# Optimization experiments

Measured on AMD Instinct MI355X. Metric: run time of the kernel, lower is better.

## Reference

```python
import jax, jax.numpy as jnp
import numpy as np

EPS = 1e-8
NUM_ITERATIONS = 3


def layer_norm(x, g, b, eps=EPS):
    m = jnp.mean(x, axis=-1, keepdims=True)
    v = jnp.mean((x - m) ** 2, axis=-1, keepdims=True)
    return (x - m) * jax.lax.rsqrt(v + eps) * g + b


def gru_cell(x, h, w_ih, w_hh, b_ih, b_hh):
    # PyTorch GRUCell: gates ordered (r, z, n)
    gi = x @ w_ih.T + b_ih  # [B*S, 3D]
    gh = h @ w_hh.T + b_hh
    i_r, i_z, i_n = jnp.split(gi, 3, axis=-1)
    h_r, h_z, h_n = jnp.split(gh, 3, axis=-1)
    r = jax.nn.sigmoid(i_r + h_r)
    z = jax.nn.sigmoid(i_z + h_z)
    n = jnp.tanh(i_n + r * h_n)
    return (1.0 - z) * n + z * h


def setup_inputs() -> dict:
    key = jax.random.key(0)
    ks = jax.random.split(key, 12)
    B, N, D, S = 64, 1024, 512, 16
    s = 1.0 / np.sqrt(D)
    return {
        "inputs": jax.random.normal(ks[0], (B, N, D), jnp.float32),
        "noise": jax.random.normal(ks[1], (B, S, D), jnp.float32),
        "slot_mu": jax.random.normal(ks[2], (1, 1, D), jnp.float32),
        "slot_log_sigma": jnp.zeros((1, 1, D), jnp.float32),
        "ln_in_g": jnp.ones((D,), jnp.float32),
        "ln_in_b": jnp.zeros((D,), jnp.float32),
        "ln_slots_g": jnp.ones((D,), jnp.float32),
        "ln_slots_b": jnp.zeros((D,), jnp.float32),
        "ln_mlp_g": jnp.ones((D,), jnp.float32),
        "ln_mlp_b": jnp.zeros((D,), jnp.float32),
        "Wq": jax.random.normal(ks[3], (D, D), jnp.float32) * s,
        "Wk": jax.random.normal(ks[4], (D, D), jnp.float32) * s,
        "Wv": jax.random.normal(ks[5], (D, D), jnp.float32) * s,
        "gru_w_ih": jax.random.normal(ks[6], (3 * D, D), jnp.float32) * s,
        "gru_w_hh": jax.random.normal(ks[7], (3 * D, D), jnp.float32) * s,
        "gru_b_ih": jnp.zeros((3 * D,), jnp.float32),
        "gru_b_hh": jnp.zeros((3 * D,), jnp.float32),
        "mlp_w1": jax.random.normal(ks[8], (D, D), jnp.float32) * s,
        "mlp_b1": jnp.zeros((D,), jnp.float32),
        "mlp_w2": jax.random.normal(ks[9], (D, D), jnp.float32) * s,
        "mlp_b2": jnp.zeros((D,), jnp.float32),
    }


def reference(inputs, noise, slot_mu, slot_log_sigma,
              ln_in_g, ln_in_b, ln_slots_g, ln_slots_b, ln_mlp_g, ln_mlp_b,
              Wq, Wk, Wv, gru_w_ih, gru_w_hh, gru_b_ih, gru_b_hh,
              mlp_w1, mlp_b1, mlp_w2, mlp_b2):
    B, N, D = inputs.shape
    S = noise.shape[1]
    scale = D ** (-0.5)

    # slot init: mu + sigma * eps
    slots = slot_mu + jnp.exp(slot_log_sigma) * noise  # [B,S,D]

    x = layer_norm(inputs, ln_in_g, ln_in_b)
    k = x @ Wk.T  # [B,N,D]
    v = x @ Wv.T

    for _ in range(NUM_ITERATIONS):
        slots_prev = slots
        sn = layer_norm(slots, ln_slots_g, ln_slots_b)
        q = sn @ Wq.T  # [B,S,D]
        attn_logits = jnp.einsum("bnd,bmd->bnm", q, k) * scale  # [B,S,N]
        attn = jax.nn.softmax(attn_logits, axis=-1)
        attn = attn / (jnp.sum(attn, axis=1, keepdims=True) + EPS)  # column-normalize over slots
        updates = jnp.einsum("bnm,bmd->bnd", attn, v)  # [B,S,D]
        slots = gru_cell(updates.reshape(-1, D), slots_prev.reshape(-1, D),
                         gru_w_ih, gru_w_hh, gru_b_ih, gru_b_hh).reshape(B, S, D)
        h = jax.nn.relu(layer_norm(slots, ln_mlp_g, ln_mlp_b) @ mlp_w1.T + mlp_b1)
        slots = slots + h @ mlp_w2.T + mlp_b2

    # proj_to_hidden is Identity (slot_dim == hidden_size); forward_dtype=float32
    return slots
```

## Files before the change

kernel.cpp:

```cpp
#include <hip/hip_runtime.h>
#include <hip/hip_bf16.h>
#include <cstdint>
#include <cstddef>


typedef __bf16 bf16x8 __attribute__((ext_vector_type(8)));
typedef float f32x4 __attribute__((ext_vector_type(4)));

__device__ __forceinline__ float bf2f(unsigned int u) {
  union { unsigned int i; float f; } v; v.i = u << 16; return v.f;
}
__device__ __forceinline__ unsigned short f2bf(float x) {
  __hip_bfloat16 h = __float2bfloat16(x);
  unsigned short u;
  __builtin_memcpy(&u, &h, 2);
  return u;
}

#define GLD16(gp, lp)                                                       \
  __builtin_amdgcn_global_load_lds(                                         \
      (const __attribute__((address_space(1))) void*)(gp),                  \
      (__attribute__((address_space(3))) void*)(lp), 16, 0, 0)


__global__ void wprep_k(const float* __restrict__ w1, const float* __restrict__ w2,
                        const float* __restrict__ wih, const float* __restrict__ bih,
                        const float* __restrict__ bhh, const float* __restrict__ mu,
                        const float* __restrict__ ls, const float* __restrict__ noise,
                        unsigned short* __restrict__ w1_bf, unsigned short* __restrict__ w2_bf,
                        unsigned short* __restrict__ wih_bf, float* __restrict__ bcat,
                        float* __restrict__ slots) {
  int blk = blockIdx.x, t = threadIdx.x;
  if (blk < 1024) {
    int i = blk * 256 + t; w1_bf[i] = f2bf(w1[i]);
  } else if (blk < 2048) {
    int i = (blk - 1024) * 256 + t; w2_bf[i] = f2bf(w2[i]);
  } else if (blk < 5120) {
    int i = (blk - 2048) * 256 + t; wih_bf[i] = f2bf(wih[i]);
  } else if (blk < 5128) {
    int j = (blk - 5120) * 256 + t;
    float v;
    if (j < 1024)      v = bih[j] + bhh[j];
    else if (j < 1536) v = bih[j];
    else               v = bhh[j - 512];
    bcat[j] = v;
  } else {
    int i = (blk - 5128) * 256 + t;
    int d = i & 511;
    slots[i] = mu[d] + expf(ls[d]) * noise[i];
  }
}

__global__ void wcat_k(const float* __restrict__ wihp, const float* __restrict__ whh,
                       unsigned short* __restrict__ out) {
  int i = blockIdx.x * 256 + threadIdx.x;
  int j = i >> 10, k = i & 1023;
  float v;
  if (j < 1024)      v = (k < 512) ? wihp[j * 512 + k] : whh[j * 512 + (k - 512)];
  else if (j < 1536) v = (k < 512) ? wihp[j * 512 + k] : 0.0f;
  else               v = (k < 512) ? 0.0f : whh[(j - 512) * 512 + (k - 512)];
  out[i] = f2bf(v);
}

__global__ __launch_bounds__(256) void tcast3_k(const float* __restrict__ Wq,
                                                const float* __restrict__ Wk,
                                                const float* __restrict__ Wv,
                                                unsigned short* __restrict__ wqT,
                                                unsigned short* __restrict__ wkT,
                                                unsigned short* __restrict__ wvT) {
  __shared__ float tt[32][33];
  const float* in = blockIdx.z == 0 ? Wq : (blockIdx.z == 1 ? Wk : Wv);
  unsigned short* out = blockIdx.z == 0 ? wqT : (blockIdx.z == 1 ? wkT : wvT);
  int c0 = blockIdx.x << 5, r0 = blockIdx.y << 5;
  int tx = threadIdx.x & 31, ty = threadIdx.x >> 5;
  #pragma unroll
  for (int i = 0; i < 4; ++i)
    tt[ty + 8 * i][tx] = in[(size_t)(r0 + ty + 8 * i) * 512 + c0 + tx];
  __syncthreads();
  #pragma unroll
  for (int i = 0; i < 4; ++i)
    out[(size_t)(c0 + ty + 8 * i) * 512 + r0 + tx] = f2bf(tt[tx][ty + 8 * i]);
}


__global__ __launch_bounds__(256) void ln_rows_k(
    const float* __restrict__ in, const float* __restrict__ g, const float* __restrict__ b,
    unsigned short* __restrict__ out, int rows) {
  int w = threadIdx.x >> 6, lane = threadIdx.x & 63;
  int row = (blockIdx.x << 2) + w;
  if (row >= rows) return;
  const float4* rp = reinterpret_cast<const float4*>(in + (size_t)row * 512);
  float4 v0 = rp[lane], v1 = rp[lane + 64];
  float s = v0.x + v0.y + v0.z + v0.w + v1.x + v1.y + v1.z + v1.w;
  float q = v0.x*v0.x + v0.y*v0.y + v0.z*v0.z + v0.w*v0.w
          + v1.x*v1.x + v1.y*v1.y + v1.z*v1.z + v1.w*v1.w;
  #pragma unroll
  for (int o = 32; o > 0; o >>= 1) { s += __shfl_xor(s, o); q += __shfl_xor(q, o); }
  float m = s * (1.0f / 512.0f);
  float rstd = rsqrtf(q * (1.0f / 512.0f) - m * m + 1e-8f);
  const float4* gp = reinterpret_cast<const float4*>(g);
  const float4* bp = reinterpret_cast<const float4*>(b);
  float4 g0 = gp[lane], g1 = gp[lane + 64];
  float4 b0 = bp[lane], b1 = bp[lane + 64];
  ushort4 o0, o1;
  o0.x = f2bf((v0.x - m) * rstd * g0.x + b0.x);
  o0.y = f2bf((v0.y - m) * rstd * g0.y + b0.y);
  o0.z = f2bf((v0.z - m) * rstd * g0.z + b0.z);
  o0.w = f2bf((v0.w - m) * rstd * g0.w + b0.w);
  o1.x = f2bf((v1.x - m) * rstd * g1.x + b1.x);
  o1.y = f2bf((v1.y - m) * rstd * g1.y + b1.y);
  o1.z = f2bf((v1.z - m) * rstd * g1.z + b1.z);
  o1.w = f2bf((v1.w - m) * rstd * g1.w + b1.w);
  ushort4* op = reinterpret_cast<ushort4*>(out + (size_t)row * 512);
  op[lane] = o0; op[lane + 64] = o1;
}


__global__ __launch_bounds__(256) void xt_k(const unsigned short* __restrict__ x,
                                            unsigned short* __restrict__ xT) {
  __shared__ unsigned short t[64][68];
  int nt = blockIdx.x, et = blockIdx.y, b = blockIdx.z;
  int r = threadIdx.x >> 3, c8 = (threadIdx.x & 7) << 3;
  #pragma unroll
  for (int p = 0; p < 2; ++p) {
    int row = r + (p << 5);
    *reinterpret_cast<uint4*>(&t[row][c8]) = *reinterpret_cast<const uint4*>(
        x + ((size_t)(b << 10) + (nt << 6) + row) * 512 + (et << 6) + c8);
  }
  __syncthreads();
  #pragma unroll
  for (int p = 0; p < 2; ++p) {
    int erow = r + (p << 5);
    ushort4 a, bb;
    #pragma unroll
    for (int j = 0; j < 4; ++j) ((unsigned short*)&a)[j] = t[c8 + j][erow];
    #pragma unroll
    for (int j = 0; j < 4; ++j) ((unsigned short*)&bb)[j] = t[c8 + 4 + j][erow];
    unsigned short* o = xT + ((size_t)(b << 9) + (et << 6) + erow) * 1024 + (nt << 6) + c8;
    *reinterpret_cast<ushort4*>(o) = a;
    *reinterpret_cast<ushort4*>(o + 4) = bb;
  }
}

__global__ __launch_bounds__(256) void gru_ln_k(
    const float* __restrict__ gates, const float* __restrict__ hp,
    const float* __restrict__ g, const float* __restrict__ b,
    float* __restrict__ sgru, unsigned short* __restrict__ lnm) {
  int w = threadIdx.x >> 6, lane = threadIdx.x & 63;
  int row = (blockIdx.x << 2) + w;
  size_t gb = (size_t)row * 2048 + (lane << 3);
  size_t hb = (size_t)row * 512 + (lane << 3);
  float rs[8], zs[8], in_[8], hn[8], hv[8], y[8];
  #pragma unroll
  for (int c = 0; c < 2; ++c) {
    *reinterpret_cast<float4*>(rs + 4*c)  = *reinterpret_cast<const float4*>(gates + gb + 4*c);
    *reinterpret_cast<float4*>(zs + 4*c)  = *reinterpret_cast<const float4*>(gates + gb + 512 + 4*c);
    *reinterpret_cast<float4*>(in_ + 4*c) = *reinterpret_cast<const float4*>(gates + gb + 1024 + 4*c);
    *reinterpret_cast<float4*>(hn + 4*c)  = *reinterpret_cast<const float4*>(gates + gb + 1536 + 4*c);
    *reinterpret_cast<float4*>(hv + 4*c)  = *reinterpret_cast<const float4*>(hp + hb + 4*c);
  }
  float s = 0.f, q = 0.f;
  #pragma unroll
  for (int j = 0; j < 8; ++j) {
    float r = 1.0f / (1.0f + expf(-rs[j]));
    float z = 1.0f / (1.0f + expf(-zs[j]));
    float n = tanhf(in_[j] + r * hn[j]);
    float h = (1.0f - z) * n + z * hv[j];
    y[j] = h; s += h; q += h * h;
  }
  #pragma unroll
  for (int o = 32; o > 0; o >>= 1) { s += __shfl_xor(s, o); q += __shfl_xor(q, o); }
  float m = s * (1.0f / 512.0f);
  float rstd = rsqrtf(q * (1.0f / 512.0f) - m * m + 1e-8f);
  const float* gg = g + (lane << 3);
  const float* bb = b + (lane << 3);
  #pragma unroll
  for (int c = 0; c < 2; ++c)
    *reinterpret_cast<float4*>(sgru + hb + 4*c) = *reinterpret_cast<const float4*>(y + 4*c);
  uint4 o4;
  unsigned int p[8];
  #pragma unroll
  for (int j = 0; j < 8; ++j) p[j] = f2bf((y[j] - m) * rstd * gg[j] + bb[j]);
  o4.x = p[0] | (p[1] << 16); o4.y = p[2] | (p[3] << 16);
  o4.z = p[4] | (p[5] << 16); o4.w = p[6] | (p[7] << 16);
  *reinterpret_cast<uint4*>(lnm + hb) = o4;
}


template<int OUTBF16>
__global__ __launch_bounds__(256) void gemm_bt(
    const unsigned short* __restrict__ A, const unsigned short* __restrict__ W,
    void* __restrict__ Cout, int M, int N, int K) {
  __shared__ unsigned short sA[2][4096];
  __shared__ unsigned short sB[2][4096];
  const int tid = threadIdx.x;
  const int lane = tid & 63, w = tid >> 6;

  int nwg = gridDim.x * gridDim.y;
  int flat = blockIdx.y * gridDim.x + blockIdx.x;
  if ((nwg & 7) == 0) { int c = nwg >> 3; flat = (flat & 7) * c + (flat >> 3); }
  const int row0 = (flat / gridDim.x) << 7;
  const int col0 = (flat % gridDim.x) << 7;

  const int wm = (w >> 1) << 6, wn = (w & 1) << 6;
  const int lrow = lane & 15, kt = (lane >> 4) << 3;
  const int srow = lane >> 2, scol = (lane & 3) << 3;

  f32x4 acc[4][4];
  #pragma unroll
  for (int m = 0; m < 4; ++m)
    #pragma unroll
    for (int n = 0; n < 4; ++n) acc[m][n] = f32x4{0.f, 0.f, 0.f, 0.f};

  auto stage = [&](int buf, int k0) {
    #pragma unroll
    for (int i = 0; i < 2; ++i) {
      int ii = w * 2 + i;
      int r = (ii << 4) + srow;
      GLD16(A + (size_t)(row0 + r) * K + k0 + scol, &sA[buf][ii * 512]);
      GLD16(W + (size_t)(col0 + r) * K + k0 + scol, &sB[buf][ii * 512]);
    }
  };

  stage(0, 0);
  const int nt = K >> 5;
  int cur = 0;
  for (int t = 0; t < nt; ++t) {
    __syncthreads();
    if (t + 1 < nt) stage(cur ^ 1, (t + 1) << 5);
    bf16x8 af[4], bfv[4];
    #pragma unroll
    for (int m = 0; m < 4; ++m)
      af[m] = *reinterpret_cast<const bf16x8*>(&sA[cur][(wm + m * 16 + lrow) * 32 + kt]);
    #pragma unroll
    for (int n = 0; n < 4; ++n)
      bfv[n] = *reinterpret_cast<const bf16x8*>(&sB[cur][(wn + n * 16 + lrow) * 32 + kt]);
    #pragma unroll
    for (int m = 0; m < 4; ++m)
      #pragma unroll
      for (int n = 0; n < 4; ++n)
        acc[m][n] = __builtin_amdgcn_mfma_f32_16x16x32_bf16(af[m], bfv[n], acc[m][n], 0, 0, 0);
    cur ^= 1;
  }

  const int rb = (lane >> 4) << 2;
  #pragma unroll
  for (int m = 0; m < 4; ++m) {
    #pragma unroll
    for (int n = 0; n < 4; ++n) {
      int col = col0 + wn + n * 16 + lrow;
      #pragma unroll
      for (int r = 0; r < 4; ++r) {
        int row = row0 + wm + m * 16 + rb + r;
        float v = acc[m][n][r];
        if (OUTBF16) ((unsigned short*)Cout)[(size_t)row * N + col] = f2bf(v);
        else ((float*)Cout)[(size_t)row * N + col] = v;
      }
    }
  }
}


__global__ __launch_bounds__(256) void q2ln_k(
    const float* __restrict__ slots, const float* __restrict__ g, const float* __restrict__ b,
    const unsigned short* __restrict__ wpt, unsigned short* __restrict__ q2,
    unsigned short* __restrict__ A2) {
  __shared__ unsigned short s_sn[16 * 520];
  __shared__ unsigned short sB[2][4096];
  const int b_ = blockIdx.y, ct = blockIdx.x;
  const int lane = threadIdx.x & 63, w = threadIdx.x >> 6;
  const int lrow = lane & 15, kt = (lane >> 4) << 3;
  const int srow = lane >> 2, scol = (lane & 3) << 3;

  const float4* gp = reinterpret_cast<const float4*>(g);
  const float4* bp = reinterpret_cast<const float4*>(b);
  float4 g0 = gp[lane], g1 = gp[lane + 64];
  float4 b0 = bp[lane], b1 = bp[lane + 64];
  #pragma unroll
  for (int rr = 0; rr < 4; ++rr) {
    int r = w * 4 + rr;
    const float4* rp = reinterpret_cast<const float4*>(slots + (size_t)(b_ * 16 + r) * 512);
    float4 v0 = rp[lane], v1 = rp[lane + 64];
    float s = v0.x + v0.y + v0.z + v0.w + v1.x + v1.y + v1.z + v1.w;
    float q = v0.x*v0.x + v0.y*v0.y + v0.z*v0.z + v0.w*v0.w
            + v1.x*v1.x + v1.y*v1.y + v1.z*v1.z + v1.w*v1.w;
    #pragma unroll
    for (int o = 32; o > 0; o >>= 1) { s += __shfl_xor(s, o); q += __shfl_xor(q, o); }
    float m = s * (1.0f / 512.0f);
    float rstd = rsqrtf(q * (1.0f / 512.0f) - m * m + 1e-8f);
    ushort4 o0, o1;
    o0.x = f2bf((v0.x - m) * rstd * g0.x + b0.x);
    o0.y = f2bf((v0.y - m) * rstd * g0.y + b0.y);
    o0.z = f2bf((v0.z - m) * rstd * g0.z + b0.z);
    o0.w = f2bf((v0.w - m) * rstd * g0.w + b0.w);
    o1.x = f2bf((v1.x - m) * rstd * g1.x + b1.x);
    o1.y = f2bf((v1.y - m) * rstd * g1.y + b1.y);
    o1.z = f2bf((v1.z - m) * rstd * g1.z + b1.z);
    o1.w = f2bf((v1.w - m) * rstd * g1.w + b1.w);
    *reinterpret_cast<ushort4*>(&s_sn[r * 520 + lane * 4]) = o0;
    *reinterpret_cast<ushort4*>(&s_sn[r * 520 + 256 + lane * 4]) = o1;
    if (ct == 0) {
      ushort4 c0, c1;
      c0.x = f2bf(v0.x); c0.y = f2bf(v0.y); c0.z = f2bf(v0.z); c0.w = f2bf(v0.w);
      c1.x = f2bf(v1.x); c1.y = f2bf(v1.y); c1.z = f2bf(v1.z); c1.w = f2bf(v1.w);
      unsigned short* a2r = A2 + (size_t)(b_ * 16 + r) * 1024 + 512;
      *reinterpret_cast<ushort4*>(a2r + lane * 4) = c0;
      *reinterpret_cast<ushort4*>(a2r + 256 + lane * 4) = c1;
    }
  }

  const unsigned short* Bb = wpt + (size_t)(ct << 7) * 512;
  auto stage = [&](int buf, int k0) {
    #pragma unroll
    for (int i = 0; i < 2; ++i) {
      int ii = w * 2 + i;
      GLD16(Bb + (size_t)((ii << 4) + srow) * 512 + k0 + scol, &sB[buf][ii * 512]);
    }
  };

  f32x4 acc[2];
  acc[0] = f32x4{0.f, 0.f, 0.f, 0.f};
  acc[1] = f32x4{0.f, 0.f, 0.f, 0.f};

  stage(0, 0);
  int cur = 0;
  for (int t = 0; t < 16; ++t) {
    __syncthreads();
    if (t + 1 < 16) stage(cur ^ 1, (t + 1) << 5);
    bf16x8 af = *reinterpret_cast<const bf16x8*>(&s_sn[lrow * 520 + (t << 5) + kt]);
    #pragma unroll
    for (int ni = 0; ni < 2; ++ni) {
      bf16x8 bfv = *reinterpret_cast<const bf16x8*>(&sB[cur][((w * 2 + ni) * 16 + lrow) * 32 + kt]);
      acc[ni] = __builtin_amdgcn_mfma_f32_16x16x32_bf16(af, bfv, acc[ni], 0, 0, 0);
    }
    cur ^= 1;
  }

  const int rb = (lane >> 4) << 2;
  #pragma unroll
  for (int ni = 0; ni < 2; ++ni) {
    int col = (ct << 7) + (w * 2 + ni) * 16 + lrow;
    #pragma unroll
    for (int r = 0; r < 4; ++r) {
      int s = rb + r;
      q2[(size_t)((b_ << 4) + s) * 512 + col] = f2bf(acc[ni][r]);
    }
  }
}


__global__ __launch_bounds__(256) void logits_k(
    const unsigned short* __restrict__ q2, const unsigned short* __restrict__ x,
    unsigned short* __restrict__ out) {
  __shared__ unsigned short sA[2][512];
  __shared__ unsigned short sB[2][4096];
  const int b = blockIdx.y, nt = blockIdx.x;
  const int lane = threadIdx.x & 63, w = threadIdx.x >> 6;
  const int lrow = lane & 15, kt = (lane >> 4) << 3;
  const int srow = lane >> 2, scol = (lane & 3) << 3;
  const unsigned short* Ab = q2 + ((size_t)b << 13);
  const unsigned short* Bb = x + (((size_t)(b << 10) + (nt << 7)) << 9);

  f32x4 acc[2];
  acc[0] = f32x4{0.f, 0.f, 0.f, 0.f};
  acc[1] = f32x4{0.f, 0.f, 0.f, 0.f};

  auto stage = [&](int buf, int k0) {
    #pragma unroll
    for (int i = 0; i < 2; ++i) {
      int ii = w * 2 + i;
      GLD16(Bb + (size_t)((ii << 4) + srow) * 512 + k0 + scol, &sB[buf][ii * 512]);
    }
    if (w == 0)
      GLD16(Ab + (size_t)srow * 512 + k0 + scol, &sA[buf][0]);
  };

  stage(0, 0);
  int cur = 0;
  for (int t = 0; t < 16; ++t) {
    __syncthreads();
    if (t + 1 < 16) stage(cur ^ 1, (t + 1) << 5);
    bf16x8 af = *reinterpret_cast<const bf16x8*>(&sA[cur][lrow * 32 + kt]);
    #pragma unroll
    for (int ni = 0; ni < 2; ++ni) {
      bf16x8 bfv = *reinterpret_cast<const bf16x8*>(&sB[cur][((w * 2 + ni) * 16 + lrow) * 32 + kt]);
      acc[ni] = __builtin_amdgcn_mfma_f32_16x16x32_bf16(af, bfv, acc[ni], 0, 0, 0);
    }
    cur ^= 1;
  }

  const int rb = (lane >> 4) << 2;
  #pragma unroll
  for (int ni = 0; ni < 2; ++ni) {
    int n = (nt << 7) + (w * 2 + ni) * 16 + lrow;
    #pragma unroll
    for (int r = 0; r < 4; ++r) {
      int s = rb + r;
      out[(size_t)((b << 4) + s) * 1024 + n] = f2bf(acc[ni][r]);
    }
  }
}


__global__ __launch_bounds__(256) void pv_sm_k(
    const unsigned short* __restrict__ logits, const unsigned short* __restrict__ xT,
    unsigned short* __restrict__ A2) {
  __shared__ float s_mi[16][2];
  __shared__ unsigned short s_at[16 * 1032];
  __shared__ unsigned short sA[2][4096];
  const int b_ = blockIdx.y, et = blockIdx.x;
  const int lane = threadIdx.x & 63, w = threadIdx.x >> 6;
  const int lrow = lane & 15, kt = (lane >> 4) << 3;
  const int srow = lane >> 2, scol = (lane & 3) << 3;
  const unsigned short* lg = logits + ((size_t)b_ << 14);

  #pragma unroll
  for (int rr = 0; rr < 4; ++rr) {
    int r = w * 4 + rr;
    const unsigned short* rp = lg + (size_t)r * 1024;
    float v[16];
    float mx = -3.4e38f;
    #pragma unroll
    for (int i = 0; i < 16; ++i) { v[i] = bf2f(rp[lane + (i << 6)]); mx = fmaxf(mx, v[i]); }
    #pragma unroll
    for (int o = 32; o > 0; o >>= 1) mx = fmaxf(mx, __shfl_xor(mx, o));
    float s = 0.f;
    #pragma unroll
    for (int i = 0; i < 16; ++i) s += __expf(v[i] - mx);
    #pragma unroll
    for (int o = 32; o > 0; o >>= 1) s += __shfl_xor(s, o);
    if (lane == 0) { s_mi[r][0] = mx; s_mi[r][1] = 1.0f / s; }
  }
  __syncthreads();

  #pragma unroll
  for (int j = 0; j < 4; ++j) {
    int c = threadIdx.x + (j << 8);
    float e[16];
    float cs = 0.f;
    #pragma unroll
    for (int s = 0; s < 16; ++s) {
      e[s] = __expf(bf2f(lg[(size_t)s * 1024 + c]) - s_mi[s][0]) * s_mi[s][1];
      cs += e[s];
    }
    float rv = 1.0f / (cs + 1e-8f);
    #pragma unroll
    for (int s = 0; s < 16; ++s) s_at[s * 1032 + c] = f2bf(e[s] * rv);
  }

  const unsigned short* Ab = xT + ((size_t)b_ << 19) + (size_t)(et << 7) * 1024;
  auto stage = [&](int buf, int k0) {
    #pragma unroll
    for (int i = 0; i < 2; ++i) {
      int ii = w * 2 + i;
      GLD16(Ab + (size_t)((ii << 4) + srow) * 1024 + k0 + scol, &sA[buf][ii * 512]);
    }
  };

  f32x4 acc[2];
  acc[0] = f32x4{0.f, 0.f, 0.f, 0.f};
  acc[1] = f32x4{0.f, 0.f, 0.f, 0.f};

  stage(0, 0);
  int cur = 0;
  for (int t = 0; t < 32; ++t) {
    __syncthreads();
    if (t + 1 < 32) stage(cur ^ 1, (t + 1) << 5);
    bf16x8 bfv = *reinterpret_cast<const bf16x8*>(&s_at[lrow * 1032 + (t << 5) + kt]);
    #pragma unroll
    for (int mi = 0; mi < 2; ++mi) {
      bf16x8 af = *reinterpret_cast<const bf16x8*>(&sA[cur][((w * 2 + mi) * 16 + lrow) * 32 + kt]);
      acc[mi] = __builtin_amdgcn_mfma_f32_16x16x32_bf16(af, bfv, acc[mi], 0, 0, 0);
    }
    cur ^= 1;
  }

  const int rb = (lane >> 4) << 2;
  const int s = lrow;
  #pragma unroll
  for (int mi = 0; mi < 2; ++mi) {
    int e0 = (et << 7) + (w * 2 + mi) * 16 + rb;
    ushort4 o;
    o.x = f2bf(acc[mi][0]); o.y = f2bf(acc[mi][1]);
    o.z = f2bf(acc[mi][2]); o.w = f2bf(acc[mi][3]);
    *reinterpret_cast<ushort4*>(&A2[(size_t)((b_ << 4) + s) * 1024 + e0]) = o;
  }
}


template<int BIAS, int RELU, int ADDSRC, int OUTBF16, int SCALE>
__global__ __launch_bounds__(256) void gemm_sm(
    const unsigned short* __restrict__ A, const unsigned short* __restrict__ W,
    const float* __restrict__ bias, const float* __restrict__ addsrc,
    void* __restrict__ Cout, int M, int N, int K, float scalev) {
  __shared__ unsigned short sA[2][2048];
  __shared__ unsigned short sB[2][2048];
  const int tid = threadIdx.x;
  const int lane = tid & 63, w = tid >> 6;

  int nwg = gridDim.x * gridDim.y;
  int flat = blockIdx.y * gridDim.x + blockIdx.x;
  if ((nwg & 7) == 0) { int c = nwg >> 3; flat = (flat & 7) * c + (flat >> 3); }
  const int row0 = (flat / gridDim.x) << 6;
  const int col0 = (flat % gridDim.x) << 6;

  const int lrow = lane & 15, kt = (lane >> 4) << 3;
  const int srow = lane >> 2, scol = (lane & 3) << 3;

  f32x4 acc[4];
  #pragma unroll
  for (int m = 0; m < 4; ++m) acc[m] = f32x4{0.f, 0.f, 0.f, 0.f};

  auto stage = [&](int buf, int k0) {
    int r = (w << 4) + srow;
    GLD16(A + (size_t)(row0 + r) * K + k0 + scol, &sA[buf][w * 512]);
    GLD16(W + (size_t)(col0 + r) * K + k0 + scol, &sB[buf][w * 512]);
  };

  stage(0, 0);
  const int nt = K >> 5;
  int cur = 0;
  for (int t = 0; t < nt; ++t) {
    __syncthreads();
    if (t + 1 < nt) stage(cur ^ 1, (t + 1) << 5);
    bf16x8 af[4], bfv;
    #pragma unroll
    for (int m = 0; m < 4; ++m)
      af[m] = *reinterpret_cast<const bf16x8*>(&sA[cur][(m * 16 + lrow) * 32 + kt]);
    bfv = *reinterpret_cast<const bf16x8*>(&sB[cur][((w << 4) + lrow) * 32 + kt]);
    #pragma unroll
    for (int m = 0; m < 4; ++m)
      acc[m] = __builtin_amdgcn_mfma_f32_16x16x32_bf16(af[m], bfv, acc[m], 0, 0, 0);
    cur ^= 1;
  }

  const int rb = (lane >> 4) << 2;
  const int col = col0 + (w << 4) + lrow;
  float bv = BIAS ? bias[col] : 0.0f;
  #pragma unroll
  for (int m = 0; m < 4; ++m) {
    #pragma unroll
    for (int r = 0; r < 4; ++r) {
      int row = row0 + m * 16 + rb + r;
      float v = acc[m][r];
      if (SCALE) v *= scalev;
      v += bv;
      if (ADDSRC) v += addsrc[(size_t)row * N + col];
      if (RELU) v = fmaxf(v, 0.0f);
      if (OUTBF16) ((unsigned short*)Cout)[(size_t)row * N + col] = f2bf(v);
      else ((float*)Cout)[(size_t)row * N + col] = v;
    }
  }
}


extern "C" void kernel_launch(void* const* d_in, const int* in_sizes, int n_in,
                              void* d_out, int out_size, void* d_ws, size_t ws_size,
                              hipStream_t stream) {
  const float* inputs  = (const float*)d_in[0];
  const float* noise   = (const float*)d_in[1];
  const float* slot_mu = (const float*)d_in[2];
  const float* slot_ls = (const float*)d_in[3];
  const float* ln_in_g = (const float*)d_in[4];
  const float* ln_in_b = (const float*)d_in[5];
  const float* ln_s_g  = (const float*)d_in[6];
  const float* ln_s_b  = (const float*)d_in[7];
  const float* ln_m_g  = (const float*)d_in[8];
  const float* ln_m_b  = (const float*)d_in[9];
  const float* Wq   = (const float*)d_in[10];
  const float* Wk   = (const float*)d_in[11];
  const float* Wv   = (const float*)d_in[12];
  const float* w_ih = (const float*)d_in[13];
  const float* w_hh = (const float*)d_in[14];
  const float* b_ih = (const float*)d_in[15];
  const float* b_hh = (const float*)d_in[16];
  const float* w1   = (const float*)d_in[17];
  const float* b1   = (const float*)d_in[18];
  const float* w2   = (const float*)d_in[19];
  const float* b2   = (const float*)d_in[20];

  const int BN = 65536, BS = 1024;

  uintptr_t base = (uintptr_t)d_ws;
  auto alloc = [&](size_t bytes) {
    void* p = (void*)base;
    base += (bytes + 255) & ~(size_t)255;
    return p;
  };
  unsigned short* x_bf    = (unsigned short*)alloc((size_t)BN * 512 * 2);
  unsigned short* xT      = (unsigned short*)alloc((size_t)64 * 512 * 1024 * 2);
  unsigned short* wqT     = (unsigned short*)alloc(512 * 512 * 2);
  unsigned short* wkT     = (unsigned short*)alloc(512 * 512 * 2);
  unsigned short* wvT     = (unsigned short*)alloc(512 * 512 * 2);
  unsigned short* wpt     = (unsigned short*)alloc(512 * 512 * 2);
  unsigned short* wih_bf  = (unsigned short*)alloc((size_t)1536 * 512 * 2);
  float*          wihp    = (float*)alloc((size_t)1536 * 512 * 4);
  unsigned short* wcat_bf = (unsigned short*)alloc((size_t)2048 * 1024 * 2);
  float*          bcat    = (float*)alloc(2048 * 4);
  unsigned short* w1_bf   = (unsigned short*)alloc(512 * 512 * 2);
  unsigned short* w2_bf   = (unsigned short*)alloc(512 * 512 * 2);
  float*          slots   = (float*)alloc((size_t)BS * 512 * 4);
  unsigned short* A2      = (unsigned short*)alloc((size_t)BS * 1024 * 2);
  unsigned short* q2_bf   = (unsigned short*)alloc((size_t)BS * 512 * 2);
  unsigned short* logits  = (unsigned short*)alloc((size_t)64 * 16 * 1024 * 2);
  float*          gates   = (float*)alloc((size_t)BS * 2048 * 4);
  float*          sgru    = (float*)alloc((size_t)BS * 512 * 4);
  unsigned short* lnm_bf  = (unsigned short*)alloc((size_t)BS * 512 * 2);
  unsigned short* h_bf    = (unsigned short*)alloc((size_t)BS * 512 * 2);
  (void)ws_size; (void)n_in; (void)in_sizes; (void)out_size;

  const float scale = 0.044194173824159216f;

  wprep_k<<<7176, 256, 0, stream>>>(w1, w2, w_ih, b_ih, b_hh, slot_mu, slot_ls, noise,
                                    w1_bf, w2_bf, wih_bf, bcat, slots);
  tcast3_k<<<dim3(16, 16, 3), 256, 0, stream>>>(Wq, Wk, Wv, wqT, wkT, wvT);
  gemm_sm<0,0,0,1,1><<<dim3(8, 8), 256, 0, stream>>>(
      wkT, wqT, nullptr, nullptr, wpt, 512, 512, 512, scale);
  gemm_bt<0><<<dim3(4, 12), 256, 0, stream>>>(
      wih_bf, wvT, wihp, 1536, 512, 512);
  wcat_k<<<8192, 256, 0, stream>>>(wihp, w_hh, wcat_bf);
  ln_rows_k<<<16384, 256, 0, stream>>>(inputs, ln_in_g, ln_in_b, x_bf, BN);
  xt_k<<<dim3(16, 8, 64), 256, 0, stream>>>(x_bf, xT);

  for (int it = 0; it < 3; ++it) {
    q2ln_k<<<dim3(4, 64), 256, 0, stream>>>(slots, ln_s_g, ln_s_b, wpt, q2_bf, A2);
    logits_k<<<dim3(8, 64), 256, 0, stream>>>(q2_bf, x_bf, logits);
    pv_sm_k<<<dim3(4, 64), 256, 0, stream>>>(logits, xT, A2);
    gemm_sm<1,0,0,0,0><<<dim3(32, 16), 256, 0, stream>>>(
        A2, wcat_bf, bcat, nullptr, gates, BS, 2048, 1024, 1.0f);
    gru_ln_k<<<256, 256, 0, stream>>>(gates, slots, ln_m_g, ln_m_b, sgru, lnm_bf);
    gemm_sm<1,1,0,1,0><<<dim3(8, 16), 256, 0, stream>>>(
        lnm_bf, w1_bf, b1, nullptr, h_bf, BS, 512, 512, 1.0f);
    float* slots_out = (it == 2) ? (float*)d_out : slots;
    gemm_sm<1,0,1,0,0><<<dim3(8, 16), 256, 0, stream>>>(
        h_bf, w2_bf, b2, sgru, slots_out, BS, 512, 512, 1.0f);
  }
}
```

Before: 344.0 us.

## Double K-tile depth to 64 in all GEMMs and write Wih·Wv directly into wcat

Every MFMA GEMM kernel now stages 64-wide K tiles instead of 32, which halves the number of barrier/stage iterations and doubles the LDS buffers. The Wih·Wv product now writes bf16 directly into the concatenated GRU weight buffer with a leading dimension. The whh halves and zero blocks of that buffer are filled in the prep kernel, which removes the fp32 intermediate and the separate wcat kernel. Larger LDS use may reduce occupancy, and the 64-wide rows may raise LDS bank conflicts.

```diff
diff --git a/kernel.cpp b/kernel.cpp
--- a/kernel.cpp
+++ b/kernel.cpp
@@ -24,12 +24,13 @@
 
 
 __global__ void wprep_k(const float* __restrict__ w1, const float* __restrict__ w2,
-                        const float* __restrict__ wih, const float* __restrict__ bih,
-                        const float* __restrict__ bhh, const float* __restrict__ mu,
-                        const float* __restrict__ ls, const float* __restrict__ noise,
+                        const float* __restrict__ wih, const float* __restrict__ whh,
+                        const float* __restrict__ bih, const float* __restrict__ bhh,
+                        const float* __restrict__ mu, const float* __restrict__ ls,
+                        const float* __restrict__ noise,
                         unsigned short* __restrict__ w1_bf, unsigned short* __restrict__ w2_bf,
-                        unsigned short* __restrict__ wih_bf, float* __restrict__ bcat,
-                        float* __restrict__ slots) {
+                        unsigned short* __restrict__ wih_bf, unsigned short* __restrict__ wcat,
+                        float* __restrict__ bcat, float* __restrict__ slots) {
   int blk = blockIdx.x, t = threadIdx.x;
   if (blk < 1024) {
     int i = blk * 256 + t; w1_bf[i] = f2bf(w1[i]);
@@ -37,29 +38,36 @@
     int i = (blk - 1024) * 256 + t; w2_bf[i] = f2bf(w2[i]);
   } else if (blk < 5120) {
     int i = (blk - 2048) * 256 + t; wih_bf[i] = f2bf(wih[i]);
-  } else if (blk < 5128) {
-    int j = (blk - 5120) * 256 + t;
+  } else if (blk < 7168) {
+    int i = (blk - 5120) * 256 + t;
+    int j = i >> 9, d = i & 511;
+    wcat[(size_t)j * 1024 + 512 + d] = f2bf(whh[(size_t)j * 512 + d]);
+  } else if (blk < 8192) {
+    int i = (blk - 7168) * 256 + t;
+    int j = i >> 9, d = i & 511;
+    wcat[(size_t)(1536 + j) * 1024 + 512 + d] = f2bf(whh[(size_t)(1024 + j) * 512 + d]);
+  } else if (blk < 10240) {
+    int i = (blk - 8192) * 256 + t;
+    if (i < 262144) {
+      int j = i >> 9, d = i & 511;
+      wcat[(size_t)(1536 + j) * 1024 + d] = 0;
+    } else {
+      int k = i - 262144;
+      int j = k >> 9, d = k & 511;
+      wcat[(size_t)(1024 + j) * 1024 + 512 + d] = 0;
+    }
+  } else if (blk < 10248) {
+    int j = (blk - 10240) * 256 + t;
     float v;
     if (j < 1024)      v = bih[j] + bhh[j];
     else if (j < 1536) v = bih[j];
     else               v = bhh[j - 512];
     bcat[j] = v;
   } else {
-    int i = (blk - 5128) * 256 + t;
+    int i = (blk - 10248) * 256 + t;
     int d = i & 511;
     slots[i] = mu[d] + expf(ls[d]) * noise[i];
   }
-}
-
-__global__ void wcat_k(const float* __restrict__ wihp, const float* __restrict__ whh,
-                       unsigned short* __restrict__ out) {
-  int i = blockIdx.x * 256 + threadIdx.x;
-  int j = i >> 10, k = i & 1023;
-  float v;
-  if (j < 1024)      v = (k < 512) ? wihp[j * 512 + k] : whh[j * 512 + (k - 512)];
-  else if (j < 1536) v = (k < 512) ? wihp[j * 512 + k] : 0.0f;
-  else               v = (k < 512) ? 0.0f : whh[(j - 512) * 512 + (k - 512)];
-  out[i] = f2bf(v);
 }
 
 __global__ __launch_bounds__(256) void tcast3_k(const float* __restrict__ Wq,
@@ -187,12 +195,11 @@
 }
 
 
-template<int OUTBF16>
-__global__ __launch_bounds__(256) void gemm_bt(
+__global__ __launch_bounds__(256) void gemm_cat(
     const unsigned short* __restrict__ A, const unsigned short* __restrict__ W,
-    void* __restrict__ Cout, int M, int N, int K) {
-  __shared__ unsigned short sA[2][4096];
-  __shared__ unsigned short sB[2][4096];
+    unsigned short* __restrict__ Cout, int M, int N, int K, int ldc) {
+  __shared__ unsigned short sA[2][8192];
+  __shared__ unsigned short sB[2][8192];
   const int tid = threadIdx.x;
   const int lane = tid & 63, w = tid >> 6;
 
@@ -204,7 +211,7 @@
 
   const int wm = (w >> 1) << 6, wn = (w & 1) << 6;
   const int lrow = lane & 15, kt = (lane >> 4) << 3;
-  const int srow = lane >> 2, scol = (lane & 3) << 3;
+  const int sr8 = lane >> 3, sc8 = (lane & 7) << 3;
 
   f32x4 acc[4][4];
   #pragma unroll
@@ -214,32 +221,35 @@
 
   auto stage = [&](int buf, int k0) {
     #pragma unroll
-    for (int i = 0; i < 2; ++i) {
-      int ii = w * 2 + i;
-      int r = (ii << 4) + srow;
-      GLD16(A + (size_t)(row0 + r) * K + k0 + scol, &sA[buf][ii * 512]);
-      GLD16(W + (size_t)(col0 + r) * K + k0 + scol, &sB[buf][ii * 512]);
+    for (int i = 0; i < 4; ++i) {
+      int ii = (w << 2) + i;
+      int r = (ii << 3) + sr8;
+      GLD16(A + (size_t)(row0 + r) * K + k0 + sc8, &sA[buf][ii * 512]);
+      GLD16(W + (size_t)(col0 + r) * K + k0 + sc8, &sB[buf][ii * 512]);
     }
   };
 
   stage(0, 0);
-  const int nt = K >> 5;
+  const int nt = K >> 6;
   int cur = 0;
   for (int t = 0; t < nt; ++t) {
     __syncthreads();
-    if (t + 1 < nt) stage(cur ^ 1, (t + 1) << 5);
-    bf16x8 af[4], bfv[4];
-    #pragma unroll
-    for (int m = 0; m < 4; ++m)
-      af[m] = *reinterpret_cast<const bf16x8*>(&sA[cur][(wm + m * 16 + lrow) * 32 + kt]);
-    #pragma unroll
-    for (int n = 0; n < 4; ++n)
-      bfv[n] = *reinterpret_cast<const bf16x8*>(&sB[cur][(wn + n * 16 + lrow) * 32 + kt]);
-    #pragma unroll
-    for (int m = 0; m < 4; ++m)
+    if (t + 1 < nt) stage(cur ^ 1, (t + 1) << 6);
+    #pragma unroll
+    for (int kk = 0; kk < 2; ++kk) {
+      bf16x8 af[4], bfv[4];
+      #pragma unroll
+      for (int m = 0; m < 4; ++m)
+        af[m] = *reinterpret_cast<const bf16x8*>(&sA[cur][(wm + m * 16 + lrow) * 64 + (kk << 5) + kt]);
       #pragma unroll
       for (int n = 0; n < 4; ++n)
-        acc[m][n] = __builtin_amdgcn_mfma_f32_16x16x32_bf16(af[m], bfv[n], acc[m][n], 0, 0, 0);
+        bfv[n] = *reinterpret_cast<const bf16x8*>(&sB[cur][(wn + n * 16 + lrow) * 64 + (kk << 5) + kt]);
+      #pragma unroll
+      for (int m = 0; m < 4; ++m)
+        #pragma unroll
+        for (int n = 0; n < 4; ++n)
+          acc[m][n] = __builtin_amdgcn_mfma_f32_16x16x32_bf16(af[m], bfv[n], acc[m][n], 0, 0, 0);
+    }
     cur ^= 1;
   }
 
@@ -252,9 +262,7 @@
       #pragma unroll
       for (int r = 0; r < 4; ++r) {
         int row = row0 + wm + m * 16 + rb + r;
-        float v = acc[m][n][r];
-        if (OUTBF16) ((unsigned short*)Cout)[(size_t)row * N + col] = f2bf(v);
-        else ((float*)Cout)[(size_t)row * N + col] = v;
+        Cout[(size_t)row * ldc + col] = f2bf(acc[m][n][r]);
       }
     }
   }
@@ -266,11 +274,11 @@
     const unsigned short* __restrict__ wpt, unsigned short* __restrict__ q2,
     unsigned short* __restrict__ A2) {
   __shared__ unsigned short s_sn[16 * 520];
-  __shared__ unsigned short sB[2][4096];
+  __shared__ unsigned short sB[2][8192];
   const int b_ = blockIdx.y, ct = blockIdx.x;
   const int lane = threadIdx.x & 63, w = threadIdx.x >> 6;
   const int lrow = lane & 15, kt = (lane >> 4) << 3;
-  const int srow = lane >> 2, scol = (lane & 3) << 3;
+  const int sr8 = lane >> 3, sc8 = (lane & 7) << 3;
 
   const float4* gp = reinterpret_cast<const float4*>(g);
   const float4* bp = reinterpret_cast<const float4*>(b);
@@ -312,9 +320,9 @@
   const unsigned short* Bb = wpt + (size_t)(ct << 7) * 512;
   auto stage = [&](int buf, int k0) {
     #pragma unroll
-    for (int i = 0; i < 2; ++i) {
-      int ii = w * 2 + i;
-      GLD16(Bb + (size_t)((ii << 4) + srow) * 512 + k0 + scol, &sB[buf][ii * 512]);
+    for (int i = 0; i < 4; ++i) {
+      int ii = (w << 2) + i;
+      GLD16(Bb + (size_t)((ii << 3) + sr8) * 512 + k0 + sc8, &sB[buf][ii * 512]);
     }
   };
 
@@ -324,14 +332,18 @@
 
   stage(0, 0);
   int cur = 0;
-  for (int t = 0; t < 16; ++t) {
+  for (int t = 0; t < 8; ++t) {
     __syncthreads();
-    if (t + 1 < 16) stage(cur ^ 1, (t + 1) << 5);
-    bf16x8 af = *reinterpret_cast<const bf16x8*>(&s_sn[lrow * 520 + (t << 5) + kt]);
-    #pragma unroll
-    for (int ni = 0; ni < 2; ++ni) {
-      bf16x8 bfv = *reinterpret_cast<const bf16x8*>(&sB[cur][((w * 2 + ni) * 16 + lrow) * 32 + kt]);
-      acc[ni] = __builtin_amdgcn_mfma_f32_16x16x32_bf16(af, bfv, acc[ni], 0, 0, 0);
+    if (t + 1 < 8) stage(cur ^ 1, (t + 1) << 6);
+    #pragma unroll
+    for (int kk = 0; kk < 2; ++kk) {
+      bf16x8 af = *reinterpret_cast<const bf16x8*>(&s_sn[lrow * 520 + (t << 6) + (kk << 5) + kt]);
+      #pragma unroll
+      for (int ni = 0; ni < 2; ++ni) {
+        bf16x8 bfv = *reinterpret_cast<const bf16x8*>(
+            &sB[cur][((w * 2 + ni) * 16 + lrow) * 64 + (kk << 5) + kt]);
+        acc[ni] = __builtin_amdgcn_mfma_f32_16x16x32_bf16(af, bfv, acc[ni], 0, 0, 0);
+      }
     }
     cur ^= 1;
   }
@@ -352,12 +364,12 @@
 __global__ __launch_bounds__(256) void logits_k(
     const unsigned short* __restrict__ q2, const unsigned short* __restrict__ x,
     unsigned short* __restrict__ out) {
-  __shared__ unsigned short sA[2][512];
-  __shared__ unsigned short sB[2][4096];
+  __shared__ unsigned short sA[2][1024];
+  __shared__ unsigned short sB[2][8192];
   const int b = blockIdx.y, nt = blockIdx.x;
   const int lane = threadIdx.x & 63, w = threadIdx.x >> 6;
   const int lrow = lane & 15, kt = (lane >> 4) << 3;
-  const int srow = lane >> 2, scol = (lane & 3) << 3;
+  const int sr8 = lane >> 3, sc8 = (lane & 7) << 3;
   const unsigned short* Ab = q2 + ((size_t)b << 13);
   const unsigned short* Bb = x + (((size_t)(b << 10) + (nt << 7)) << 9);
 
@@ -367,24 +379,31 @@
 
   auto stage = [&](int buf, int k0) {
     #pragma unroll
-    for (int i = 0; i < 2; ++i) {
-      int ii = w * 2 + i;
-      GLD16(Bb + (size_t)((ii << 4) + srow) * 512 + k0 + scol, &sB[buf][ii * 512]);
-    }
-    if (w == 0)
-      GLD16(Ab + (size_t)srow * 512 + k0 + scol, &sA[buf][0]);
+    for (int i = 0; i < 4; ++i) {
+      int ii = (w << 2) + i;
+      GLD16(Bb + (size_t)((ii << 3) + sr8) * 512 + k0 + sc8, &sB[buf][ii * 512]);
+    }
+    if (w == 0) {
+      #pragma unroll
+      for (int i = 0; i < 2; ++i)
+        GLD16(Ab + (size_t)((i << 3) + sr8) * 512 + k0 + sc8, &sA[buf][i * 512]);
+    }
   };
 
   stage(0, 0);
   int cur = 0;
-  for (int t = 0; t < 16; ++t) {
+  for (int t = 0; t < 8; ++t) {
     __syncthreads();
-    if (t + 1 < 16) stage(cur ^ 1, (t + 1) << 5);
-    bf16x8 af = *reinterpret_cast<const bf16x8*>(&sA[cur][lrow * 32 + kt]);
-    #pragma unroll
-    for (int ni = 0; ni < 2; ++ni) {
-      bf16x8 bfv = *reinterpret_cast<const bf16x8*>(&sB[cur][((w * 2 + ni) * 16 + lrow) * 32 + kt]);
-      acc[ni] = __builtin_amdgcn_mfma_f32_16x16x32_bf16(af, bfv, acc[ni], 0, 0, 0);
+    if (t + 1 < 8) stage(cur ^ 1, (t + 1) << 6);
+    #pragma unroll
+    for (int kk = 0; kk < 2; ++kk) {
+      bf16x8 af = *reinterpret_cast<const bf16x8*>(&sA[cur][lrow * 64 + (kk << 5) + kt]);
+      #pragma unroll
+      for (int ni = 0; ni < 2; ++ni) {
+        bf16x8 bfv = *reinterpret_cast<const bf16x8*>(
+            &sB[cur][((w * 2 + ni) * 16 + lrow) * 64 + (kk << 5) + kt]);
+        acc[ni] = __builtin_amdgcn_mfma_f32_16x16x32_bf16(af, bfv, acc[ni], 0, 0, 0);
+      }
     }
     cur ^= 1;
   }
@@ -407,11 +426,11 @@
     unsigned short* __restrict__ A2) {
   __shared__ float s_mi[16][2];
   __shared__ unsigned short s_at[16 * 1032];
-  __shared__ unsigned short sA[2][4096];
+  __shared__ unsigned short sA[2][8192];
   const int b_ = blockIdx.y, et = blockIdx.x;
   const int lane = threadIdx.x & 63, w = threadIdx.x >> 6;
   const int lrow = lane & 15, kt = (lane >> 4) << 3;
-  const int srow = lane >> 2, scol = (lane & 3) << 3;
+  const int sr8 = lane >> 3, sc8 = (lane & 7) << 3;
   const unsigned short* lg = logits + ((size_t)b_ << 14);
 
   #pragma unroll
@@ -451,9 +470,9 @@
   const unsigned short* Ab = xT + ((size_t)b_ << 19) + (size_t)(et << 7) * 1024;
   auto stage = [&](int buf, int k0) {
     #pragma unroll
-    for (int i = 0; i < 2; ++i) {
-      int ii = w * 2 + i;
-      GLD16(Ab + (size_t)((ii << 4) + srow) * 1024 + k0 + scol, &sA[buf][ii * 512]);
+    for (int i = 0; i < 4; ++i) {
+      int ii = (w << 2) + i;
+      GLD16(Ab + (size_t)((ii << 3) + sr8) * 1024 + k0 + sc8, &sA[buf][ii * 512]);
     }
   };
 
@@ -463,14 +482,18 @@
 
   stage(0, 0);
   int cur = 0;
-  for (int t = 0; t < 32; ++t) {
+  for (int t = 0; t < 16; ++t) {
     __syncthreads();
-    if (t + 1 < 32) stage(cur ^ 1, (t + 1) << 5);
-    bf16x8 bfv = *reinterpret_cast<const bf16x8*>(&s_at[lrow * 1032 + (t << 5) + kt]);
-    #pragma unroll
-    for (int mi = 0; mi < 2; ++mi) {
-      bf16x8 af = *reinterpret_cast<const bf16x8*>(&sA[cur][((w * 2 + mi) * 16 + lrow) * 32 + kt]);
-      acc[mi] = __builtin_amdgcn_mfma_f32_16x16x32_bf16(af, bfv, acc[mi], 0, 0, 0);
+    if (t + 1 < 16) stage(cur ^ 1, (t + 1) << 6);
+    #pragma unroll
+    for (int kk = 0; kk < 2; ++kk) {
+      bf16x8 bfv = *reinterpret_cast<const bf16x8*>(&s_at[lrow * 1032 + (t << 6) + (kk << 5) + kt]);
+      #pragma unroll
+      for (int mi = 0; mi < 2; ++mi) {
+        bf16x8 af = *reinterpret_cast<const bf16x8*>(
+            &sA[cur][((w * 2 + mi) * 16 + lrow) * 64 + (kk << 5) + kt]);
+        acc[mi] = __builtin_amdgcn_mfma_f32_16x16x32_bf16(af, bfv, acc[mi], 0, 0, 0);
+      }
     }
     cur ^= 1;
   }
@@ -493,8 +516,8 @@
     const unsigned short* __restrict__ A, const unsigned short* __restrict__ W,
     const float* __restrict__ bias, const float* __restrict__ addsrc,
     void* __restrict__ Cout, int M, int N, int K, float scalev) {
-  __shared__ unsigned short sA[2][2048];
-  __shared__ unsigned short sB[2][2048];
+  __shared__ unsigned short sA[2][4096];
+  __shared__ unsigned short sB[2][4096];
   const int tid = threadIdx.x;
   const int lane = tid & 63, w = tid >> 6;
 
@@ -505,32 +528,39 @@
   const int col0 = (flat % gridDim.x) << 6;
 
   const int lrow = lane & 15, kt = (lane >> 4) << 3;
-  const int srow = lane >> 2, scol = (lane & 3) << 3;
+  const int sr8 = lane >> 3, sc8 = (lane & 7) << 3;
 
   f32x4 acc[4];
   #pragma unroll
   for (int m = 0; m < 4; ++m) acc[m] = f32x4{0.f, 0.f, 0.f, 0.f};
 
   auto stage = [&](int buf, int k0) {
-    int r = (w << 4) + srow;
-    GLD16(A + (size_t)(row0 + r) * K + k0 + scol, &sA[buf][w * 512]);
-    GLD16(W + (size_t)(col0 + r) * K + k0 + scol, &sB[buf][w * 512]);
+    #pragma unroll
+    for (int i = 0; i < 2; ++i) {
+      int ii = (w << 1) + i;
+      int r = (ii << 3) + sr8;
+      GLD16(A + (size_t)(row0 + r) * K + k0 + sc8, &sA[buf][ii * 512]);
+      GLD16(W + (size_t)(col0 + r) * K + k0 + sc8, &sB[buf][ii * 512]);
+    }
   };
 
   stage(0, 0);
-  const int nt = K >> 5;
+  const int nt = K >> 6;
   int cur = 0;
   for (int t = 0; t < nt; ++t) {
     __syncthreads();
-    if (t + 1 < nt) stage(cur ^ 1, (t + 1) << 5);
-    bf16x8 af[4], bfv;
-    #pragma unroll
-    for (int m = 0; m < 4; ++m)
-      af[m] = *reinterpret_cast<const bf16x8*>(&sA[cur][(m * 16 + lrow) * 32 + kt]);
-    bfv = *reinterpret_cast<const bf16x8*>(&sB[cur][((w << 4) + lrow) * 32 + kt]);
-    #pragma unroll
-    for (int m = 0; m < 4; ++m)
-      acc[m] = __builtin_amdgcn_mfma_f32_16x16x32_bf16(af[m], bfv, acc[m], 0, 0, 0);
+    if (t + 1 < nt) stage(cur ^ 1, (t + 1) << 6);
+    #pragma unroll
+    for (int kk = 0; kk < 2; ++kk) {
+      bf16x8 bfv = *reinterpret_cast<const bf16x8*>(
+          &sB[cur][((w << 4) + lrow) * 64 + (kk << 5) + kt]);
+      #pragma unroll
+      for (int m = 0; m < 4; ++m) {
+        bf16x8 af = *reinterpret_cast<const bf16x8*>(
+            &sA[cur][(m * 16 + lrow) * 64 + (kk << 5) + kt]);
+        acc[m] = __builtin_amdgcn_mfma_f32_16x16x32_bf16(af, bfv, acc[m], 0, 0, 0);
+      }
+    }
     cur ^= 1;
   }
 
@@ -594,7 +624,6 @@
   unsigned short* wvT     = (unsigned short*)alloc(512 * 512 * 2);
   unsigned short* wpt     = (unsigned short*)alloc(512 * 512 * 2);
   unsigned short* wih_bf  = (unsigned short*)alloc((size_t)1536 * 512 * 2);
-  float*          wihp    = (float*)alloc((size_t)1536 * 512 * 4);
   unsigned short* wcat_bf = (unsigned short*)alloc((size_t)2048 * 1024 * 2);
   float*          bcat    = (float*)alloc(2048 * 4);
   unsigned short* w1_bf   = (unsigned short*)alloc(512 * 512 * 2);
@@ -611,14 +640,14 @@
 
   const float scale = 0.044194173824159216f;
 
-  wprep_k<<<7176, 256, 0, stream>>>(w1, w2, w_ih, b_ih, b_hh, slot_mu, slot_ls, noise,
-                                    w1_bf, w2_bf, wih_bf, bcat, slots);
+  wprep_k<<<12296, 256, 0, stream>>>(w1, w2, w_ih, w_hh, b_ih, b_hh,
+                                     slot_mu, slot_ls, noise,
+                                     w1_bf, w2_bf, wih_bf, wcat_bf, bcat, slots);
   tcast3_k<<<dim3(16, 16, 3), 256, 0, stream>>>(Wq, Wk, Wv, wqT, wkT, wvT);
   gemm_sm<0,0,0,1,1><<<dim3(8, 8), 256, 0, stream>>>(
       wkT, wqT, nullptr, nullptr, wpt, 512, 512, 512, scale);
-  gemm_bt<0><<<dim3(4, 12), 256, 0, stream>>>(
-      wih_bf, wvT, wihp, 1536, 512, 512);
-  wcat_k<<<8192, 256, 0, stream>>>(wihp, w_hh, wcat_bf);
+  gemm_cat<<<dim3(4, 12), 256, 0, stream>>>(
+      wih_bf, wvT, wcat_bf, 1536, 512, 512, 1024);
   ln_rows_k<<<16384, 256, 0, stream>>>(inputs, ln_in_g, ln_in_b, x_bf, BN);
   xt_k<<<dim3(16, 8, 64), 256, 0, stream>>>(x_bf, xT);
 
```

Measured after the change: 331.4 us. 3.7% less time.
